# Kernel tuning notes

Hardware: AMD Instinct MI355X
Metric: run time of the kernel (lower is better)

## Reference

```python
import math
import jax, jax.numpy as jnp
import numpy as np

IN_FEATURES = 4096
OUT_FEATURES = 4096
BLOCK_SIZE = 256
N_TOKENS = 8192


def _butterfly_layout(out_blocks, in_blocks, butterfly_size):
    # sum of log2(n) butterfly factors with all-ones 2x2 twiddles:
    # block (o, i) is active iff o == i or o == i ^ 2^k for some factor k
    log_n = int(math.log2(butterfly_size))
    idx = np.arange(butterfly_size)
    layout = np.zeros((butterfly_size, butterfly_size), dtype=bool)
    layout[idx, idx] = True
    for k in range(log_n):
        layout[idx ^ (1 << k), idx] = True
    if out_blocks > butterfly_size:
        layout = np.tile(layout, (out_blocks // butterfly_size, 1))
    if in_blocks > butterfly_size:
        layout = np.tile(layout, (1, in_blocks // butterfly_size))
    return layout


def _flat_indices(layout):
    # For each output block, flat indices into [num_in_blocks * active_blocks_per_input]
    # selecting which per-input weight blocks are summed (embedding_bag mode='sum').
    num_out, num_in = layout.shape
    abpi = int(layout.sum(0)[0])
    abpo = int(layout.sum(1)[0])
    rank = np.cumsum(layout, axis=0) - 1  # rank of output o among active outputs of input i
    o_idx, i_idx = np.nonzero(layout)     # row-major -> grouped by output block
    flat = i_idx * abpi + rank[o_idx, i_idx]
    return flat.reshape(num_out, abpo).astype(np.int32), abpi


def setup_inputs() -> dict:
    key = jax.random.key(0)
    k1, k2 = jax.random.split(key)
    in_blocks = IN_FEATURES // BLOCK_SIZE
    out_blocks = OUT_FEATURES // BLOCK_SIZE
    butterfly_size = min(IN_FEATURES, OUT_FEATURES) // BLOCK_SIZE  # 16
    layout = _butterfly_layout(out_blocks, in_blocks, butterfly_size)
    flat_idx, abpi = _flat_indices(layout)  # abpi = log2(16)+1 = 5
    std = math.sqrt(2.0 / (5 * min(IN_FEATURES, OUT_FEATURES)))
    weight = jax.random.normal(k1, (IN_FEATURES, abpi, BLOCK_SIZE), dtype=jnp.float32) * std
    x = jax.random.normal(k2, (N_TOKENS, IN_FEATURES), dtype=jnp.float32)
    return {"x": x, "weight": weight, "flat_indices": jnp.asarray(flat_idx)}


def reference(x, weight, flat_indices):
    # x: [B, in_features]; weight: [in_features, abpi, block_size]
    in_features, abpi, bs = weight.shape
    num_in = in_features // bs
    B = x.shape[0]
    xb = x.reshape(B, num_in, bs)                  # [B, g, k]
    w = weight.reshape(num_in, bs, abpi, bs)       # [g, k, a, o]
    # per-input-block partial output blocks: [g, a, B, o]
    blocks = jnp.einsum('bgk,gkao->gabo', xb, w)
    blocks = blocks.reshape(num_in * abpi, B, bs)
    # gather + sum active blocks per output block (embedding_bag mode='sum')
    out_blocks = blocks[flat_indices].sum(axis=1)  # [num_out_blocks, B, bs]
    out = jnp.transpose(out_blocks, (1, 0, 2)).reshape(B, -1)  # [B, out_features]
    return out
```

## Files before the change

kernel.cpp:

```cpp
#include <hip/hip_runtime.h>
#include <stdint.h>

#define N_TOK 8192
#define IN_F 4096
#define OUT_F 4096
#define BS 256
#define ABPI 5
#define NFLAT 80

typedef __attribute__((ext_vector_type(8))) short short8;
typedef __attribute__((ext_vector_type(4))) float floatx4;
typedef __attribute__((ext_vector_type(4))) unsigned short ushort4v;

__device__ __forceinline__ unsigned short f2bf(float f) {
  union { float f; unsigned int u; } v; v.f = f;
  unsigned int r = v.u + 0x7FFFu + ((v.u >> 16) & 1u);
  return (unsigned short)(r >> 16);
}

__device__ __forceinline__ void async16(const void* g, void* l) {
  __builtin_amdgcn_global_load_lds((const __attribute__((address_space(1))) void*)g,
                                   (__attribute__((address_space(3))) void*)l, 16, 0, 0);
}

__global__ void cvt_x_kernel(const float4* __restrict__ x, ushort4v* __restrict__ xb) {
  int idx = blockIdx.x * 256 + threadIdx.x;
  const int stride = 2048 * 256;
  #pragma unroll
  for (int i = 0; i < 16; ++i, idx += stride) {
    float4 a = x[idx];
    ushort4v o;
    o[0] = f2bf(a.x); o[1] = f2bf(a.y); o[2] = f2bf(a.z); o[3] = f2bf(a.w);
    xb[idx] = o;
  }
}

__global__ void cvt_w_kernel(const float* __restrict__ w, unsigned short* __restrict__ wt) {
  __shared__ unsigned short tile[64][68];
  int b = blockIdx.x;
  int fi = b >> 4;
  int t  = b & 15;
  int k0 = (t >> 2) * 64, o0 = (t & 3) * 64;
  int g = fi / ABPI, a = fi % ABPI;
  int tid = threadIdx.x;
  int tr = tid >> 4, tc = tid & 15;
  #pragma unroll
  for (int i = 0; i < 4; ++i) {
    int k = k0 + i * 16 + tr;
    const float* src = w + (size_t)(g * 256 + k) * (ABPI * BS) + a * BS + o0 + tc * 4;
    float4 v = *(const float4*)src;
    tile[tc * 4 + 0][i * 16 + tr] = f2bf(v.x);
    tile[tc * 4 + 1][i * 16 + tr] = f2bf(v.y);
    tile[tc * 4 + 2][i * 16 + tr] = f2bf(v.z);
    tile[tc * 4 + 3][i * 16 + tr] = f2bf(v.w);
  }
  __syncthreads();
  #pragma unroll
  for (int i = 0; i < 4; ++i) {
    int o = i * 16 + tr;
    unsigned short* dst = wt + (size_t)fi * (BS * BS) + (size_t)(o0 + o) * BS + k0 + tc * 4;
    *(ushort4v*)dst = *(const ushort4v*)&tile[o][tc * 4];
  }
}


#define BM 256
#define BN 256
#define BK 64
#define ABYTES 32768
#define BUFBYTES 65536
#define SMEM_TOTAL 131072

__device__ __forceinline__ void ld_half_A(const char* p, int c0, int c1, short8 (&af)[4][2]) {
  #pragma unroll
  for (int mt = 0; mt < 4; ++mt) {
    const char* q = p + mt * 2048;
    af[mt][0] = *(const short8*)(q + c0);
    af[mt][1] = *(const short8*)(q + c1);
  }
}

__device__ __forceinline__ void ld_pair_B(const char* p, int c0, int c1, short8 (&bf)[2][2]) {
  #pragma unroll
  for (int nt = 0; nt < 2; ++nt) {
    const char* q = p + nt * 2048;
    bf[nt][0] = *(const short8*)(q + c0);
    bf[nt][1] = *(const short8*)(q + c1);
  }
}

__device__ __forceinline__ void mma16(const short8 (&af)[4][2], const short8 (&bf)[2][2],
                                      floatx4 (&acc)[8][4], int mb, int nb) {
  #pragma unroll
  for (int mt = 0; mt < 4; ++mt)
    #pragma unroll
    for (int nt = 0; nt < 2; ++nt) {
      acc[mb + mt][nb + nt] =
          __builtin_amdgcn_mfma_f32_16x16x32_bf16(af[mt][0], bf[nt][0], acc[mb + mt][nb + nt], 0, 0, 0);
      acc[mb + mt][nb + nt] =
          __builtin_amdgcn_mfma_f32_16x16x32_bf16(af[mt][1], bf[nt][1], acc[mb + mt][nb + nt], 0, 0, 0);
    }
}

#define KTILE(tt, Ab, Bb, Asd, Bsd, DOSTAGE, LAST)                              \
  do {                                                                          \
    if (DOSTAGE) {                                                              \
      const int u = (tt) + 1, su = u >> 2, ku = (u & 3) * 64;                   \
      const int uA = gcol[su] + ku, uB = wbase[su] + ku;                        \
      async16(pA0 + uA, (Asd)         + tid16);                                 \
      async16(pA1 + uA, (Asd) +  8192 + tid16);                                 \
      async16(pA2 + uA, (Asd) + 16384 + tid16);                                 \
      async16(pA3 + uA, (Asd) + 24576 + tid16);                                 \
      async16(pB0 + uB, (Bsd)         + tid16);                                 \
      async16(pB1 + uB, (Bsd) +  8192 + tid16);                                 \
      async16(pB2 + uB, (Bsd) + 16384 + tid16);                                 \
      async16(pB3 + uB, (Bsd) + 24576 + tid16);                                 \
    }                                                                           \
    ld_half_A((Ab) + rAb, c0, c1, af);                      \
    ld_pair_B((Bb) + rBb, c0, c1, bf01);                                 \
    ld_pair_B((Bb) + rBb + 4096, c0, c1, bf23);                          \
    asm volatile("s_waitcnt lgkmcnt(4)" ::: "memory");    \
    __builtin_amdgcn_sched_barrier(0);                                          \
    __builtin_amdgcn_s_setprio(1);                                              \
    mma16(af, bf01, acc, 0, 0);                    \
    __builtin_amdgcn_s_setprio(0);                                              \
    asm volatile("s_waitcnt lgkmcnt(0)" ::: "memory");                          \
    __builtin_amdgcn_sched_barrier(0);                                          \
    __builtin_amdgcn_s_setprio(1);                                              \
    mma16(af, bf23, acc, 0, 2);                                         \
    __builtin_amdgcn_s_setprio(0);                                              \
    __builtin_amdgcn_sched_barrier(0);            \
    ld_half_A((Ab) + rAb + 8192, c0, c1, af);             \
    asm volatile("s_waitcnt lgkmcnt(0)" ::: "memory");                          \
    __builtin_amdgcn_sched_barrier(0);                                          \
    __builtin_amdgcn_s_setprio(1);                                              \
    mma16(af, bf23, acc, 4, 2);                                         \
    mma16(af, bf01, acc, 4, 0);                        \
    __builtin_amdgcn_s_setprio(0);                                              \
    if (DOSTAGE) {                                                              \
      asm volatile("s_waitcnt vmcnt(0)" ::: "memory");    \
      __builtin_amdgcn_sched_barrier(0);                                        \
      __builtin_amdgcn_s_barrier();                  \
    } else if (!(LAST)) {                                                       \
      __builtin_amdgcn_s_barrier();                                             \
    }                                                                           \
  } while (0)

__global__ __launch_bounds__(512, 2)
void bfly_gemm(const unsigned short* __restrict__ xb,
               const unsigned short* __restrict__ wt,
               const int* __restrict__ fidx,
               float* __restrict__ out)
{
  extern __shared__ __align__(16) char smem[];
  char* const b0A = smem;
  char* const b0B = b0A + ABYTES;
  char* const b1A = smem + BUFBYTES;
  char* const b1B = b1A + ABYTES;

  const int tid = threadIdx.x;
  const int bx  = blockIdx.x;
  const int swz = (bx & 7) * 64 + (bx >> 3);
  const int ob  = swz >> 5;
  const int mt0 = swz & 31;
  const int m0  = mt0 * BM;
  const int n0g = ob * 256;

  int wbase[ABPI], gcol[ABPI];
  #pragma unroll
  for (int s = 0; s < ABPI; ++s) {
    int fi = __builtin_amdgcn_readfirstlane(fidx[ob * ABPI + s]);
    wbase[s] = fi * (BS * BS);
    gcol[s]  = (fi / ABPI) * BS;
  }

  const int sr = tid >> 3;
  const int sc = tid & 7;
  const int lc = sc ^ (sr & 7);
  const int tid16 = tid * 16;
  const unsigned short* pA0 = xb + (size_t)(m0 +   0 + sr) * IN_F + lc * 8;
  const unsigned short* pA1 = xb + (size_t)(m0 +  64 + sr) * IN_F + lc * 8;
  const unsigned short* pA2 = xb + (size_t)(m0 + 128 + sr) * IN_F + lc * 8;
  const unsigned short* pA3 = xb + (size_t)(m0 + 192 + sr) * IN_F + lc * 8;
  const unsigned short* pB0 = wt + (  0 + sr) * BS + lc * 8;
  const unsigned short* pB1 = wt + ( 64 + sr) * BS + lc * 8;
  const unsigned short* pB2 = wt + (128 + sr) * BS + lc * 8;
  const unsigned short* pB3 = wt + (192 + sr) * BS + lc * 8;

  const int lane = tid & 63;
  const int wv   = tid >> 6;
  const int wm   = (wv >> 2) * 128;
  const int wn   = (wv & 3) * 64;
  const int lrow = lane & 15;
  const int quad = lane >> 4;
  const int rAb  = (wm + lrow) * 128;
  const int rBb  = (wn + lrow) * 128;
  const int c0   = ((quad)     ^ (lrow & 7)) * 16;
  const int c1   = ((quad + 4) ^ (lrow & 7)) * 16;

  short8 af[4][2], bf01[2][2], bf23[2][2];
  floatx4 acc[8][4] = {};

  {
    const int uA0 = gcol[0], uB0 = wbase[0];
    async16(pA0 + uA0, b0A         + tid16);
    async16(pA1 + uA0, b0A +  8192 + tid16);
    async16(pA2 + uA0, b0A + 16384 + tid16);
    async16(pA3 + uA0, b0A + 24576 + tid16);
    async16(pB0 + uB0, b0B         + tid16);
    async16(pB1 + uB0, b0B +  8192 + tid16);
    async16(pB2 + uB0, b0B + 16384 + tid16);
    async16(pB3 + uB0, b0B + 24576 + tid16);
    asm volatile("s_waitcnt vmcnt(0)" ::: "memory");
    __builtin_amdgcn_sched_barrier(0);
    __builtin_amdgcn_s_barrier();
  }

  #pragma unroll 1
  for (int j = 0; j < 9; ++j) {
    const int t = j * 2;
    KTILE(t,     b0A, b0B, b1A, b1B, true, false);
    KTILE(t + 1, b1A, b1B, b0A, b0B, true, false);
  }
  KTILE(18, b0A, b0B, b1A, b1B, true, false);
  KTILE(19, b1A, b1B, b0A, b0B, false, true);

  #pragma unroll
  for (int m = 0; m < 8; ++m) {
    const int row = m0 + wm + (m >> 2) * 64 + (m & 3) * 16 + quad * 4;
    #pragma unroll
    for (int n = 0; n < 4; ++n) {
      const int col = n0g + wn + n * 16 + lrow;
      float* po = out + (size_t)row * OUT_F + col;
      #pragma unroll
      for (int r = 0; r < 4; ++r)
        po[(size_t)r * OUT_F] = acc[m][n][r];
    }
  }
}

extern "C" void kernel_launch(void* const* d_in, const int* in_sizes, int n_in,
                              void* d_out, int out_size, void* d_ws, size_t ws_size,
                              hipStream_t stream) {
  const float* x  = (const float*)d_in[0];
  const float* w  = (const float*)d_in[1];
  const int* fidx = (const int*)d_in[2];
  float* out = (float*)d_out;

  unsigned short* xb = (unsigned short*)d_ws;
  unsigned short* wt = xb + (size_t)N_TOK * IN_F;

  static int smem_set = 0;
  if (!smem_set) {
    hipFuncSetAttribute((const void*)bfly_gemm,
                        hipFuncAttributeMaxDynamicSharedMemorySize, SMEM_TOTAL);
    smem_set = 1;
  }

  cvt_x_kernel<<<2048, 256, 0, stream>>>((const float4*)x, (ushort4v*)xb);
  cvt_w_kernel<<<NFLAT * 16, 256, 0, stream>>>(w, wt);
  bfly_gemm<<<16 * 32, 512, SMEM_TOTAL, stream>>>(xb, wt, fidx, out);
}
```

Measured before the change: 327.9 us.

## Interleave async tile loads with MFMA phases and prefetch A two tiles ahead

Restructures the K-loop so the global-to-LDS async loads for B (next tile) and A (two tiles ahead, reusing the current A buffer once its rows are consumed) are split into quarters and issued between the four MFMA phases. Wave-level barriers separate the phases. Only a partial vmcnt wait is used at each tile end, so loads stay in flight across iterations. The goal is to hide global memory latency and spread load issue over the compute. The cost is many more s_barrier calls per tile and tighter correctness dependencies on buffer reuse timing.

```diff
diff --git a/kernel.cpp b/kernel.cpp
--- a/kernel.cpp
+++ b/kernel.cpp
@@ -71,6 +71,12 @@
 #define BUFBYTES 65536
 #define SMEM_TOTAL 131072
 
+#define SB() __builtin_amdgcn_sched_barrier(0)
+#define PRIO1() __builtin_amdgcn_s_setprio(1)
+#define PRIO0() __builtin_amdgcn_s_setprio(0)
+#define BARRIER() __builtin_amdgcn_s_barrier()
+#define LGKM0() do { asm volatile("s_waitcnt lgkmcnt(0)" ::: "memory"); SB(); } while (0)
+
 __device__ __forceinline__ void ld_half_A(const char* p, int c0, int c1, short8 (&af)[4][2]) {
   #pragma unroll
   for (int mt = 0; mt < 4; ++mt) {
@@ -102,48 +108,39 @@
     }
 }
 
-#define KTILE(tt, Ab, Bb, Asd, Bsd, DOSTAGE, LAST)                              \
+#define KTILE(Ab, Bb, Bsd, uB, uA2, STB, STA, END)                              \
   do {                                                                          \
-    if (DOSTAGE) {                                                              \
-      const int u = (tt) + 1, su = u >> 2, ku = (u & 3) * 64;                   \
-      const int uA = gcol[su] + ku, uB = wbase[su] + ku;                        \
-      async16(pA0 + uA, (Asd)         + tid16);                                 \
-      async16(pA1 + uA, (Asd) +  8192 + tid16);                                 \
-      async16(pA2 + uA, (Asd) + 16384 + tid16);                                 \
-      async16(pA3 + uA, (Asd) + 24576 + tid16);                                 \
-      async16(pB0 + uB, (Bsd)         + tid16);                                 \
-      async16(pB1 + uB, (Bsd) +  8192 + tid16);                                 \
-      async16(pB2 + uB, (Bsd) + 16384 + tid16);                                 \
-      async16(pB3 + uB, (Bsd) + 24576 + tid16);                                 \
-    }                                                                           \
-    ld_half_A((Ab) + rAb, c0, c1, af);                      \
-    ld_pair_B((Bb) + rBb, c0, c1, bf01);                                 \
-    ld_pair_B((Bb) + rBb + 4096, c0, c1, bf23);                          \
-    asm volatile("s_waitcnt lgkmcnt(4)" ::: "memory");    \
-    __builtin_amdgcn_sched_barrier(0);                                          \
-    __builtin_amdgcn_s_setprio(1);                                              \
-    mma16(af, bf01, acc, 0, 0);                    \
-    __builtin_amdgcn_s_setprio(0);                                              \
-    asm volatile("s_waitcnt lgkmcnt(0)" ::: "memory");                          \
-    __builtin_amdgcn_sched_barrier(0);                                          \
-    __builtin_amdgcn_s_setprio(1);                                              \
-    mma16(af, bf23, acc, 0, 2);                                         \
-    __builtin_amdgcn_s_setprio(0);                                              \
-    __builtin_amdgcn_sched_barrier(0);            \
-    ld_half_A((Ab) + rAb + 8192, c0, c1, af);             \
-    asm volatile("s_waitcnt lgkmcnt(0)" ::: "memory");                          \
-    __builtin_amdgcn_sched_barrier(0);                                          \
-    __builtin_amdgcn_s_setprio(1);                                              \
-    mma16(af, bf23, acc, 4, 2);                                         \
-    mma16(af, bf01, acc, 4, 0);                        \
-    __builtin_amdgcn_s_setprio(0);                                              \
-    if (DOSTAGE) {                                                              \
-      asm volatile("s_waitcnt vmcnt(0)" ::: "memory");    \
-      __builtin_amdgcn_sched_barrier(0);                                        \
-      __builtin_amdgcn_s_barrier();                  \
-    } else if (!(LAST)) {                                                       \
-      __builtin_amdgcn_s_barrier();                                             \
-    }                                                                           \
+                     \
+    if (STB) { async16(pB0 + (uB), (Bsd)         + tid16);                      \
+               async16(pB1 + (uB), (Bsd) +  8192 + tid16); }                    \
+    ld_half_A((Ab) + rAb,        c0, c1, af);                                   \
+    ld_pair_B((Bb) + rBb,        c0, c1, bf01);                                 \
+    ld_pair_B((Bb) + rBb + 4096, c0, c1, bf23);                                 \
+    SB(); BARRIER(); LGKM0();                                                   \
+    PRIO1(); mma16(af, bf01, acc, 0, 0); PRIO0();                               \
+    BARRIER();                                                                  \
+                                          \
+    if (STB) { async16(pB2 + (uB), (Bsd) + 16384 + tid16);                      \
+               async16(pB3 + (uB), (Bsd) + 24576 + tid16); }                    \
+    SB(); BARRIER();                                                            \
+    PRIO1(); mma16(af, bf23, acc, 0, 2); PRIO0();                               \
+    BARRIER();                                                                  \
+     \
+    if (STA) { async16(pA0 + (uA2), (Ab)         + tid16);                      \
+               async16(pA2 + (uA2), (Ab) + 16384 + tid16); }                    \
+    ld_half_A((Ab) + rAb + 8192, c0, c1, af);                                   \
+    SB(); BARRIER(); LGKM0();                                                   \
+    PRIO1(); mma16(af, bf23, acc, 4, 2); PRIO0();                               \
+    BARRIER();                                                                  \
+                                            \
+    if (STA) { async16(pA1 + (uA2), (Ab) +  8192 + tid16);                      \
+               async16(pA3 + (uA2), (Ab) + 24576 + tid16); }                    \
+    SB(); BARRIER();                                                            \
+    PRIO1(); mma16(af, bf01, acc, 4, 0); PRIO0();                               \
+    if ((END) == 2)      { asm volatile("s_waitcnt vmcnt(4)" ::: "memory");     \
+                           SB(); BARRIER(); }                                   \
+    else if ((END) == 1) { asm volatile("s_waitcnt vmcnt(0)" ::: "memory");     \
+                           SB(); BARRIER(); }                                   \
   } while (0)
 
 __global__ __launch_bounds__(512, 2)
@@ -202,7 +199,7 @@
   floatx4 acc[8][4] = {};
 
   {
-    const int uA0 = gcol[0], uB0 = wbase[0];
+    const int uA0 = gcol[0], uB0 = wbase[0], uA1 = gcol[0] + 64;
     async16(pA0 + uA0, b0A         + tid16);
     async16(pA1 + uA0, b0A +  8192 + tid16);
     async16(pA2 + uA0, b0A + 16384 + tid16);
@@ -211,19 +208,32 @@
     async16(pB1 + uB0, b0B +  8192 + tid16);
     async16(pB2 + uB0, b0B + 16384 + tid16);
     async16(pB3 + uB0, b0B + 24576 + tid16);
-    asm volatile("s_waitcnt vmcnt(0)" ::: "memory");
-    __builtin_amdgcn_sched_barrier(0);
-    __builtin_amdgcn_s_barrier();
+    SB();
+    async16(pA0 + uA1, b1A         + tid16);
+    async16(pA1 + uA1, b1A +  8192 + tid16);
+    async16(pA2 + uA1, b1A + 16384 + tid16);
+    async16(pA3 + uA1, b1A + 24576 + tid16);
+    asm volatile("s_waitcnt vmcnt(4)" ::: "memory");
+    SB();
+    BARRIER();
   }
 
   #pragma unroll 1
-  for (int j = 0; j < 9; ++j) {
-    const int t = j * 2;
-    KTILE(t,     b0A, b0B, b1A, b1B, true, false);
-    KTILE(t + 1, b1A, b1B, b0A, b0B, true, false);
-  }
-  KTILE(18, b0A, b0B, b1A, b1B, true, false);
-  KTILE(19, b1A, b1B, b0A, b0B, false, true);
+  for (int g = 0; g < 4; ++g) {
+    const int wbg = wbase[g], gcg = gcol[g];
+    const int wbn = wbase[g + 1], gcn = gcol[g + 1];
+    KTILE(b0A, b0B, b1B, wbg +  64, gcg + 128, 1, 1, 2);
+    KTILE(b1A, b1B, b0B, wbg + 128, gcg + 192, 1, 1, 2);
+    KTILE(b0A, b0B, b1B, wbg + 192, gcn,       1, 1, 2);
+    KTILE(b1A, b1B, b0B, wbn,       gcn +  64, 1, 1, 2);
+  }
+  {
+    const int wbg = wbase[4], gcg = gcol[4];
+    KTILE(b0A, b0B, b1B, wbg +  64, gcg + 128, 1, 1, 2);
+    KTILE(b1A, b1B, b0B, wbg + 128, gcg + 192, 1, 1, 2);
+    KTILE(b0A, b0B, b1B, wbg + 192, 0,         1, 0, 1);
+    KTILE(b1A, b1B, b0B, 0,         0,         0, 0, 0);
+  }
 
   #pragma unroll
   for (int m = 0; m < 8; ++m) {
```

Result: no change. 328.4 us (+0.1%).
